# Performance work log

Measured on AMD Instinct MI355X. Metric: run time of the kernel, lower is better.

Reference implementation:

```python
import jax, jax.numpy as jnp
import numpy as np
import math

G_GRAPHS = 32   # graphs per batch
NPG = 2048      # nodes per graph
DEG = 8         # avg degree
IN_DIM = 128
HID = 128

def _lin(k, fi, fo):
    return jax.random.normal(k, (fi, fo), jnp.float32) / np.sqrt(fi).astype(np.float32)

def setup_inputs():
    key = jax.random.key(0)
    ks = jax.random.split(key, 32)
    Nt = G_GRAPHS * NPG
    Epg = NPG * DEG
    E = G_GRAPHS * Epg
    x = jax.random.normal(ks[0], (Nt, IN_DIM), jnp.float32)
    src = jax.random.randint(ks[1], (E,), 0, NPG)
    dst = jax.random.randint(ks[2], (E,), 0, NPG)
    off = (jnp.arange(E) // Epg) * NPG  # keep edges within their graph block
    edge_index = jnp.stack([src + off, dst + off]).astype(jnp.int32)
    batch = (jnp.arange(Nt) // NPG).astype(jnp.int32)
    p = {}
    dims = [(IN_DIM, HID), (HID, HID), (HID, HID), (HID, HID)]
    for i, (fi, fo) in enumerate(dims, 1):
        p['Wl%d' % i] = _lin(ks[3 * i], fi, fo)
        p['bl%d' % i] = jnp.zeros((fo,), jnp.float32)
        p['Wr%d' % i] = _lin(ks[3 * i + 1], fi, fo)
    for j in (1, 2):  # SAGPooling score GNN (GraphConv hidden->1)
        p['Prel%d' % j] = _lin(ks[15 + 2 * j], HID, 1)
        p['prb%d' % j] = jnp.zeros((1,), jnp.float32)
        p['Proot%d' % j] = _lin(ks[16 + 2 * j], HID, 1)
    p['W5'] = _lin(ks[24], HID, 64); p['b5'] = jnp.zeros((64,), jnp.float32)
    p['W6'] = _lin(ks[25], 64, 2);  p['b6'] = jnp.zeros((2,), jnp.float32)
    return dict(x=x, edge_index=edge_index, batch=batch, npg=NPG, **p)

def reference(x, edge_index, batch, npg,
              Wl1, bl1, Wr1, Wl2, bl2, Wr2, Wl3, bl3, Wr3, Wl4, bl4, Wr4,
              Prel1, prb1, Proot1, Prel2, prb2, Proot2, W5, b5, W6, b6):
    src, dst = edge_index[0], edge_index[1]
    Nt = x.shape[0]
    Gn = Nt // npg

    def sage(h, em, Wl, bl, Wr):
        # SAGEConv (mean aggr): lin_l(mean_j x_j) + lin_r(x_root)
        s = jax.ops.segment_sum(h[src] * em[:, None], dst, num_segments=Nt)
        c = jax.ops.segment_sum(em, dst, num_segments=Nt)
        return (s / jnp.maximum(c, 1.0)[:, None]) @ Wl + bl + h @ Wr

    def pool(h, em, nm, k, Prel, prb, Proot):
        # SAGPooling: score = GraphConv(h) (add aggr), top-k per graph, x *= tanh(score)
        s = jax.ops.segment_sum(h[src] * em[:, None], dst, num_segments=Nt)
        score = (s @ Prel + h @ Proot + prb)[:, 0]
        smr = jnp.where(nm > 0, score, -1e30).reshape(Gn, npg)
        _, idx = jax.lax.top_k(smr, k)
        newm = jnp.zeros((Gn, npg), h.dtype).at[jnp.arange(Gn)[:, None], idx].set(1.0).reshape(-1)
        h = h * jnp.tanh(score)[:, None] * newm[:, None]
        em = em * newm[src] * newm[dst]  # filter_adj: keep edges with both ends kept
        return h, em, newm

    em = jnp.ones(src.shape, x.dtype)
    nm = jnp.ones((Nt,), x.dtype)
    h = jax.nn.relu(sage(x, em, Wl1, bl1, Wr1))
    h = jax.nn.relu(sage(h, em, Wl2, bl2, Wr2))
    k1 = math.ceil(0.5 * npg)
    h, em, nm = pool(h, em, nm, k1, Prel1, prb1, Proot1)
    h = jax.nn.relu(sage(h, em, Wl3, bl3, Wr3)) * nm[:, None]
    h = jax.nn.relu(sage(h, em, Wl4, bl4, Wr4)) * nm[:, None]
    k2 = math.ceil(0.5 * k1)
    h, em, nm = pool(h, em, nm, k2, Prel2, prb2, Proot2)
    # global mean pool over surviving nodes
    sums = jax.ops.segment_sum(h, batch, num_segments=Gn)
    cnt = jax.ops.segment_sum(nm, batch, num_segments=Gn)
    g = sums / jnp.maximum(cnt, 1.0)[:, None]
    g = jax.nn.relu(g @ W5 + b5)
    return jax.nn.log_softmax(g @ W6 + b6, axis=1)
```

## Files before the change

kernel.cpp:

```cpp
#include <hip/hip_runtime.h>
#include <hip/hip_bf16.h>
#include <math.h>

#define NT   65536
#define NPGC 2048
#define NG   32
#define NE   524288
#define HID  128
#define K1   1024
#define K2   512

typedef short short8 __attribute__((ext_vector_type(8)));
typedef float f32x4  __attribute__((ext_vector_type(4)));

__device__ __forceinline__ float bf2f(unsigned short u) {
    union { unsigned int i; float f; } v; v.i = ((unsigned int)u) << 16; return v.f;
}
__device__ __forceinline__ unsigned short f2bf(float f) {
    union { float f; unsigned int i; } v; v.f = f;
    unsigned int x = v.i;
    return (unsigned short)((x + 0x7fffu + ((x >> 16) & 1u)) >> 16);
}
__device__ __forceinline__ void split2(float v, unsigned short& hi, unsigned short& lo) {
    unsigned int b = __float_as_uint(v);
    hi = (unsigned short)(b >> 16);
    float rem = v - __uint_as_float(b & 0xFFFF0000u);
    lo = (unsigned short)(__float_as_uint(rem) >> 16);
}

__global__ void k_detect(const unsigned short* __restrict__ x, int* __restrict__ flag) {
    __shared__ int cnt;
    if (threadIdx.x == 0) cnt = 0;
    __syncthreads();
    int sane = 0;
#pragma unroll
    for (int j = 0; j < 16; ++j) {
        unsigned short u = x[threadIdx.x * 16 + j];
        int e = (u >> 7) & 0xFF;
        if (e > 0x60 && e < 0xA0) sane++;
    }
    atomicAdd(&cnt, sane);
    __syncthreads();
    if (threadIdx.x == 0) *flag = (cnt > 3686) ? 1 : 0;
}

struct CvtDesc { const void* src[22]; int n[22]; int off[22]; };

__global__ void k_cvt(CvtDesc d, float* __restrict__ wts, const int* __restrict__ flag) {
    int t = blockIdx.y;
    int n = d.n[t];
    bool isbf = (*flag != 0);
    const unsigned short* sb = (const unsigned short*)d.src[t];
    const float* sf = (const float*)d.src[t];
    float* o = wts + d.off[t];
    for (int i = blockIdx.x * blockDim.x + threadIdx.x; i < n; i += gridDim.x * blockDim.x)
        o[i] = isbf ? bf2f(sb[i]) : sf[i];
}

__global__ void k_packW(const float* __restrict__ wts, int4 oWl, int4 oWr,
                        unsigned short* __restrict__ Wpack,
                        int* __restrict__ rowc, int* __restrict__ fill) {
    int idx = blockIdx.x * 256 + threadIdx.x;
    if (idx < NT) { rowc[idx] = 0; fill[idx] = 0; }
    if (idx >= 4 * 8 * 8 * 64 * 8) return;
    int L    = idx >> 15;
    int rem  = idx & 32767;
    int ct   = rem >> 12;
    int rem2 = rem & 4095;
    int ks   = rem2 >> 9;
    int rem3 = rem2 & 511;
    int lane = rem3 >> 3;
    int j    = rem3 & 7;
    int k   = ks * 32 + (lane >> 4) * 8 + j;
    int col = ct * 16 + (lane & 15);
    int ol = (L == 0) ? oWl.x : (L == 1) ? oWl.y : (L == 2) ? oWl.z : oWl.w;
    int orr = (L == 0) ? oWr.x : (L == 1) ? oWr.y : (L == 2) ? oWr.z : oWr.w;
    float w = (k < 128) ? wts[ol + k * 128 + col] : wts[orr + (k - 128) * 128 + col];
    unsigned short hi = f2bf(w);
    unsigned short lo = f2bf(w - bf2f(hi));
    int base = L * 65536 + (ct * 8 + ks) * 512 + lane * 8 + j;
    Wpack[base]         = hi;
    Wpack[base + 32768] = lo;
}

__global__ void k_load_x(const void* __restrict__ x, float* __restrict__ out,
                         const int* __restrict__ flag, int n4,
                         float* __restrict__ nm, const int* __restrict__ dstE,
                         int* __restrict__ rowc) {
    int i = blockIdx.x * blockDim.x + threadIdx.x;
    if (i < NT) nm[i] = 1.0f;
    if (i < NE) atomicAdd(&rowc[dstE[i]], 1);
    if (i >= n4) return;
    if (*flag) {
        ushort4 v = ((const ushort4*)x)[i];
        float4 o;
        o.x = bf2f(v.x); o.y = bf2f(v.y); o.z = bf2f(v.z); o.w = bf2f(v.w);
        ((float4*)out)[i] = o;
    }
}

__global__ void k_scan1(const int* __restrict__ cnt, int* __restrict__ rp, int* __restrict__ bsum,
                        float* __restrict__ invc) {
    __shared__ int s[256];
    int t = threadIdx.x;
    int i = blockIdx.x * 256 + t;
    int v = cnt[i];
    invc[i] = 1.0f / fmaxf((float)v, 1.0f);
    s[t] = v;
    __syncthreads();
    for (int off = 1; off < 256; off <<= 1) {
        int a = (t >= off) ? s[t - off] : 0;
        __syncthreads();
        s[t] += a;
        __syncthreads();
    }
    rp[i] = s[t] - v;
    if (t == 255) bsum[blockIdx.x] = s[255];
}

__global__ void k_scan23(int* __restrict__ rp, const int* __restrict__ bsum) {
    __shared__ int s[256];
    int t = threadIdx.x;
    s[t] = bsum[t];
    __syncthreads();
    for (int off = 1; off < 256; off <<= 1) {
        int a = (t >= off) ? s[t - off] : 0;
        __syncthreads();
        s[t] += a;
        __syncthreads();
    }
    int boffv = s[blockIdx.x] - bsum[blockIdx.x];
    int i = blockIdx.x * 256 + t;
    rp[i] += boffv;
    if (i == 0) rp[NT] = NE;
}

__global__ void k_scatter(const int* __restrict__ src, const int* __restrict__ dst,
                          const int* __restrict__ rp, int* __restrict__ fill, int* __restrict__ col) {
    int e = blockIdx.x * blockDim.x + threadIdx.x;
    if (e < NE) {
        int d = dst[e];
        int p = rp[d] + atomicAdd(&fill[d], 1);
        col[p] = src[e];
    }
}

__global__ void k_invc(const float* __restrict__ nm, const int* __restrict__ rp,
                       const int* __restrict__ col, float* __restrict__ invc,
                       const int* __restrict__ act) {
    int n = act[blockIdx.x * 256 + threadIdx.x];
    int beg = rp[n], end = rp[n + 1];
    float c = 0.f;
    for (int e = beg; e < end; ++e) c += nm[col[e]];
    invc[n] = 1.0f / fmaxf(c, 1.0f);
}

__device__ __forceinline__ int lds_sw(int node, int k) {
    int g = k >> 3;
    int go = g ^ (node & 7);
    return node * 128 + go * 8 + (k & 7);
}

template<bool HAS_TS, bool COMPACT>
__device__ __forceinline__ void sage_body(
    const float* __restrict__ h, const float* __restrict__ ts,
    const float* __restrict__ nm, const float* __restrict__ invc,
    const int* __restrict__ rp, const int* __restrict__ col,
    const unsigned short* __restrict__ Wp,
    unsigned short* Ahi, unsigned short* Alo,
    unsigned short* Bhi, unsigned short* Blo,
    int n0, const int* __restrict__ actb, int tid, f32x4 acc[2][2])
{
    int lane = tid & 63, w = tid >> 6;
    int lrow = lane & 15, quad = lane >> 4;

    float4 rootv[4]; float roots[4];
#pragma unroll
    for (int i = 0; i < 4; ++i) {
        int idx = i * 256 + tid;
        int node = idx >> 5;
        int f2 = (idx & 31) * 4;
        int gn = COMPACT ? actb[node] : n0 + node;
        rootv[i] = *(const float4*)&h[(size_t)gn * HID + f2];
        roots[i] = HAS_TS ? ts[gn] : 1.0f;
    }

    int gnode = tid >> 5;
    int f = (tid & 31) * 4;
#pragma unroll
    for (int pass = 0; pass < 4; ++pass) {
        int node = pass * 8 + gnode;
        int gn = COMPACT ? actb[node] : n0 + node;
        float ax = 0.f, ay = 0.f, az = 0.f, aw = 0.f;
        bool active = COMPACT ? true : (nm[gn] > 0.f);
        if (active) {
            int beg = rp[gn], end = rp[gn + 1];
            int ecl = end - 1;
            for (int e0 = beg; e0 < end; e0 += 8) {
                int sj[8];
#pragma unroll
                for (int j = 0; j < 8; ++j) {
                    int e = (e0 + j < end) ? e0 + j : ecl;
                    sj[j] = col[e];
                }
                float4 vj[8];
#pragma unroll
                for (int j = 0; j < 8; ++j)
                    vj[j] = *(const float4*)&h[(size_t)sj[j] * HID + f];
#pragma unroll
                for (int j = 0; j < 8; ++j) {
                    float cj = (e0 + j < end) ? (HAS_TS ? ts[sj[j]] : 1.0f) : 0.0f;
                    ax += vj[j].x * cj;
                    ay += vj[j].y * cj;
                    az += vj[j].z * cj;
                    aw += vj[j].w * cj;
                }
            }
        }
        float inv = invc[gn];
        ushort4 hi4, lo4;
        split2(ax * inv, hi4.x, lo4.x);
        split2(ay * inv, hi4.y, lo4.y);
        split2(az * inv, hi4.z, lo4.z);
        split2(aw * inv, hi4.w, lo4.w);
        int a = lds_sw(node, f);
        *(ushort4*)&Ahi[a] = hi4;
        *(ushort4*)&Alo[a] = lo4;
    }

#pragma unroll
    for (int i = 0; i < 4; ++i) {
        int idx = i * 256 + tid;
        int node = idx >> 5;
        int f2 = (idx & 31) * 4;
        float sc = roots[i];
        ushort4 hi4, lo4;
        split2(rootv[i].x * sc, hi4.x, lo4.x);
        split2(rootv[i].y * sc, hi4.y, lo4.y);
        split2(rootv[i].z * sc, hi4.z, lo4.z);
        split2(rootv[i].w * sc, hi4.w, lo4.w);
        int a = lds_sw(node, f2);
        *(ushort4*)&Bhi[a] = hi4;
        *(ushort4*)&Blo[a] = lo4;
    }
    __syncthreads();

#pragma unroll
    for (int ks = 0; ks < 8; ++ks) {
        const unsigned short* Hb = (ks < 4) ? Ahi : Bhi;
        const unsigned short* Lb = (ks < 4) ? Alo : Blo;
        short8 bh[2], blo[2];
#pragma unroll
        for (int c = 0; c < 2; ++c) {
            int ct = 2 * w + c;
            bh[c]  = *(const short8*)&Wp[(ct * 8 + ks) * 512 + lane * 8];
            blo[c] = *(const short8*)&Wp[32768 + (ct * 8 + ks) * 512 + lane * 8];
        }
        int kb = (ks & 3) * 32 + quad * 8;
#pragma unroll
        for (int st = 0; st < 2; ++st) {
            int a = lds_sw(st * 16 + lrow, kb);
            short8 ah = *(const short8*)&Hb[a];
            short8 al = *(const short8*)&Lb[a];
#pragma unroll
            for (int c = 0; c < 2; ++c) {
                acc[st][c] = __builtin_amdgcn_mfma_f32_16x16x32_bf16(ah, bh[c],  acc[st][c], 0, 0, 0);
                acc[st][c] = __builtin_amdgcn_mfma_f32_16x16x32_bf16(al, bh[c],  acc[st][c], 0, 0, 0);
                acc[st][c] = __builtin_amdgcn_mfma_f32_16x16x32_bf16(ah, blo[c], acc[st][c], 0, 0, 0);
            }
        }
    }
}

template<bool COMPACT>
__device__ __forceinline__ void map_block(int b, int& graph, int& tile) {
    if (COMPACT) { graph = (b & 7) * 4 + (b >> 8); tile = (b >> 3) & 31; }
    else         { graph = (b & 7) * 4 + (b >> 9); tile = (b >> 3) & 63; }
}

template<bool HAS_TS, bool COMPACT>
__global__ void __launch_bounds__(256, 4) k_sage_plain(
    const float* __restrict__ h, const void* __restrict__ xraw, const int* __restrict__ flag,
    const float* __restrict__ ts,
    const float* __restrict__ nm, const float* __restrict__ invc,
    const int* __restrict__ rp, const int* __restrict__ col,
    const unsigned short* __restrict__ Wp, const float* __restrict__ bl,
    float* __restrict__ out, const int* __restrict__ act)
{
    __shared__ unsigned short Ahi[32 * 128];
    __shared__ unsigned short Alo[32 * 128];
    __shared__ unsigned short Bhi[32 * 128];
    __shared__ unsigned short Blo[32 * 128];
    int tid = threadIdx.x;
    int graph, tile;
    map_block<COMPACT>(blockIdx.x, graph, tile);
    int n0 = graph * NPGC + tile * 32;
    const int* actb = COMPACT ? (act + graph * K1 + tile * 32) : nullptr;
    int lane = tid & 63, w = tid >> 6;
    int lrow = lane & 15, quad = lane >> 4;
    f32x4 acc[2][2] = {};

    const float* hh = h;
    if (!COMPACT && xraw && *flag == 0) hh = (const float*)xraw;

    sage_body<HAS_TS, COMPACT>(hh, ts, nm, invc, rp, col, Wp, Ahi, Alo, Bhi, Blo, n0, actb, tid, acc);

#pragma unroll
    for (int c = 0; c < 2; ++c) {
        int colg = (2 * w + c) * 16 + lrow;
        float bias = bl[colg];
#pragma unroll
        for (int st = 0; st < 2; ++st) {
#pragma unroll
            for (int rr = 0; rr < 4; ++rr) {
                int nl = st * 16 + quad * 4 + rr;
                int node = COMPACT ? actb[nl] : n0 + nl;
                float val = fmaxf(acc[st][c][rr] + bias, 0.f);
                if (!COMPACT) val *= nm[node];
                out[(size_t)node * HID + colg] = val;
            }
        }
    }
}

template<bool HAS_TS, bool COMPACT>
__global__ void __launch_bounds__(256, 4) k_sage_dots(
    const float* __restrict__ h, const float* __restrict__ ts,
    const float* __restrict__ nm, const float* __restrict__ invc,
    const int* __restrict__ rp, const int* __restrict__ col,
    const unsigned short* __restrict__ Wp, const float* __restrict__ bl,
    float* __restrict__ out,
    const float* __restrict__ Prel, const float* __restrict__ Proot,
    float* __restrict__ q, float* __restrict__ r, const int* __restrict__ act)
{
    __shared__ unsigned short Ahi[32 * 128];
    __shared__ unsigned short Alo[32 * 128];
    __shared__ unsigned short Bhi[32 * 128];
    __shared__ unsigned short Blo[32 * 128];
    int tid = threadIdx.x;
    int graph, tile;
    map_block<COMPACT>(blockIdx.x, graph, tile);
    int n0 = graph * NPGC + tile * 32;
    const int* actb = COMPACT ? (act + graph * K1 + tile * 32) : nullptr;
    int lane = tid & 63, w = tid >> 6;
    int lrow = lane & 15, quad = lane >> 4;
    f32x4 acc[2][2] = {};

    sage_body<HAS_TS, COMPACT>(h, ts, nm, invc, rp, col, Wp, Ahi, Alo, Bhi, Blo, n0, actb, tid, acc);

    float qp[2][4] = {}, rp_[2][4] = {};
#pragma unroll
    for (int c = 0; c < 2; ++c) {
        int colg = (2 * w + c) * 16 + lrow;
        float bias = bl[colg];
        float pq = Prel[colg], pr = Proot[colg];
#pragma unroll
        for (int st = 0; st < 2; ++st) {
#pragma unroll
            for (int rr = 0; rr < 4; ++rr) {
                int nl = st * 16 + quad * 4 + rr;
                int node = COMPACT ? actb[nl] : n0 + nl;
                float val = fmaxf(acc[st][c][rr] + bias, 0.f);
                if (!COMPACT) val *= nm[node];
                out[(size_t)node * HID + colg] = val;
                qp[st][rr] += val * pq;
                rp_[st][rr] += val * pr;
            }
        }
    }
#pragma unroll
    for (int st = 0; st < 2; ++st)
#pragma unroll
        for (int rr = 0; rr < 4; ++rr) {
#pragma unroll
            for (int m = 1; m < 16; m <<= 1) {
                qp[st][rr]  += __shfl_xor(qp[st][rr],  m, 64);
                rp_[st][rr] += __shfl_xor(rp_[st][rr], m, 64);
            }
        }
    __syncthreads();
    float* qa = (float*)Ahi;
    if (tid < 64) qa[tid] = 0.f;
    __syncthreads();
    if (lrow == 0) {
#pragma unroll
        for (int st = 0; st < 2; ++st)
#pragma unroll
            for (int rr = 0; rr < 4; ++rr) {
                int nl = st * 16 + quad * 4 + rr;
                atomicAdd(&qa[nl], qp[st][rr]);
                atomicAdd(&qa[32 + nl], rp_[st][rr]);
            }
    }
    __syncthreads();
    if (tid < 32) {
        int node = COMPACT ? actb[tid] : n0 + tid;
        q[node] = qa[tid];
        r[node] = qa[32 + tid];
    }
}

__global__ void k_score(const float* __restrict__ q, const float* __restrict__ r,
                        const float* __restrict__ prb,
                        const int* __restrict__ rp, const int* __restrict__ col,
                        float* __restrict__ score) {
    int n = blockIdx.x * 256 + threadIdx.x;
    int beg = rp[n], end = rp[n + 1];
    float s = 0.f;
    for (int e = beg; e < end; ++e) s += q[col[e]];
    score[n] = s + r[n] + prb[0];
}

__global__ void k_score_act(const float* __restrict__ q, const float* __restrict__ r,
                            const float* __restrict__ prb,
                            const int* __restrict__ rp, const int* __restrict__ col,
                            float* __restrict__ score, const int* __restrict__ act) {
    int n = act[blockIdx.x * 256 + threadIdx.x];
    int beg = rp[n], end = rp[n + 1];
    float s = 0.f;
    for (int e = beg; e < end; ++e) s += q[col[e]];
    score[n] = s + r[n] + prb[0];
}

template<bool ZQ>
__global__ void __launch_bounds__(256) k_topk(const float* __restrict__ score,
                                              float* __restrict__ nm,
                                              float* __restrict__ tval, int k,
                                              int* __restrict__ act,
                                              float* __restrict__ q) {
    __shared__ unsigned int u[NPGC];
    __shared__ int hist[256];
    __shared__ int scanb[257];
    __shared__ int wtot[4];
    __shared__ int wtot2[4];
    __shared__ unsigned int s_byte;
    __shared__ int s_kk;
    int tid = threadIdx.x;
    int lane = tid & 63, wv = tid >> 6;
    int base = blockIdx.x * NPGC;

    for (int j = tid; j < NPGC; j += 256) {
        float sc = (nm[base + j] > 0.f) ? score[base + j] : -1e30f;
        unsigned int v = __float_as_uint(sc);
        v = (v & 0x80000000u) ? ~v : (v | 0x80000000u);
        u[j] = v;
    }
    hist[tid] = 0;
    if (tid == 0) scanb[256] = 0;
    __syncthreads();

    unsigned int prefix = 0;
    int kk = k;
#pragma unroll
    for (int round = 0; round < 4; ++round) {
        int shift = 24 - 8 * round;
        unsigned int pmask = (round == 0) ? 0u : (0xFFFFFFFFu << (32 - 8 * round));
        for (int j = tid; j < NPGC; j += 256) {
            unsigned int v = u[j];
            if ((v & pmask) == prefix) atomicAdd(&hist[(v >> shift) & 0xFF], 1);
        }
        __syncthreads();
        int s = hist[tid];
#pragma unroll
        for (int off = 1; off < 64; off <<= 1) {
            int t = __shfl_down(s, off, 64);
            s += (lane + off < 64) ? t : 0;
        }
        if (lane == 0) wtot[wv] = s;
        __syncthreads();
        int add = 0;
#pragma unroll
        for (int w2 = 1; w2 < 4; ++w2) add += (wv + w2 < 4) ? wtot[wv + w2] : 0;
        s += add;
        scanb[tid] = s;
        __syncthreads();
        int above = scanb[tid + 1];
        if (s >= kk && above < kk) { s_byte = (unsigned int)tid; s_kk = kk - above; }
        hist[tid] = 0;
        __syncthreads();
        prefix |= (s_byte << shift);
        kk = s_kk;
    }
    unsigned int thr = prefix;

    int j0 = tid * 8;
    int cnt = 0;
#pragma unroll
    for (int j = 0; j < 8; ++j) cnt += (u[j0 + j] == thr);
    int s = cnt;
#pragma unroll
    for (int off = 1; off < 64; off <<= 1) {
        int t = __shfl_up(s, off, 64);
        s += (lane >= off) ? t : 0;
    }
    if (lane == 63) wtot[wv] = s;
    __syncthreads();
    int add = 0;
#pragma unroll
    for (int w2 = 0; w2 < 4; ++w2) add += (w2 < wv) ? wtot[w2] : 0;
    int rank = s - cnt + add;

    unsigned int keepmask = 0u;
    int myrank = rank;
    int kcnt = 0;
#pragma unroll
    for (int j = 0; j < 8; ++j) {
        unsigned int v = u[j0 + j];
        bool kp;
        if (v > thr) kp = true;
        else if (v == thr) { kp = (myrank < kk); myrank++; }
        else kp = false;
        keepmask |= (kp ? 1u : 0u) << j;
        kcnt += kp ? 1 : 0;
    }
    int s2 = kcnt;
#pragma unroll
    for (int off = 1; off < 64; off <<= 1) {
        int t2 = __shfl_up(s2, off, 64);
        s2 += (lane >= off) ? t2 : 0;
    }
    if (lane == 63) wtot2[wv] = s2;
    __syncthreads();
    int pos = s2 - kcnt;
#pragma unroll
    for (int w2 = 0; w2 < 4; ++w2) pos += (w2 < wv) ? wtot2[w2] : 0;
    int* actg = act + blockIdx.x * k;
#pragma unroll
    for (int j = 0; j < 8; ++j) {
        bool kp = (keepmask >> j) & 1u;
        int n = base + j0 + j;
        nm[n]   = kp ? 1.0f : 0.0f;
        tval[n] = kp ? tanhf(score[n]) : 0.0f;
        if (kp)      { actg[pos++] = n; }
        else if (ZQ) { q[n] = 0.0f; }
    }
}

__global__ void k_gsum(const float* __restrict__ h, const float* __restrict__ t,
                       const int* __restrict__ act, float* __restrict__ g) {
    int b = blockIdx.x;
    int graph = b >> 2, part = b & 3;
    int f = threadIdx.x & 127, sub = threadIdx.x >> 7;
    int base = graph * K2 + part * 128 + sub * 64;
    float acc = 0.f;
#pragma unroll 4
    for (int n = 0; n < 64; ++n) {
        int gn = act[base + n];
        acc += h[(size_t)gn * HID + f] * t[gn];
    }
    atomicAdd(&g[graph * HID + f], acc);
}

__global__ void k_mlp(const float* __restrict__ g,
                      const float* __restrict__ W5,
                      const float* __restrict__ b5, const float* __restrict__ W6,
                      const float* __restrict__ b6, void* __restrict__ out,
                      const int* __restrict__ flag) {
    __shared__ float g5[64];
    __shared__ float ls[2];
    int graph = blockIdx.x, j = threadIdx.x;
    const float ic = 1.0f / (float)K2;
    float acc = b5[j];
    for (int f = 0; f < HID; ++f)
        acc += (g[graph * HID + f] * ic) * W5[f * 64 + j];
    g5[j] = fmaxf(acc, 0.f);
    __syncthreads();
    if (j < 2) {
        float l = b6[j];
        for (int t = 0; t < 64; ++t) l += g5[t] * W6[t * 2 + j];
        ls[j] = l;
    }
    __syncthreads();
    if (j == 0) {
        float a = ls[0], b = ls[1];
        float mx = fmaxf(a, b);
        float lse = mx + logf(expf(a - mx) + expf(b - mx));
        if (*flag) {
            ((unsigned short*)out)[graph * 2 + 0] = f2bf(a - lse);
            ((unsigned short*)out)[graph * 2 + 1] = f2bf(b - lse);
        } else {
            ((float*)out)[graph * 2 + 0] = a - lse;
            ((float*)out)[graph * 2 + 1] = b - lse;
        }
    }
}

extern "C" void kernel_launch(void* const* d_in, const int* in_sizes, int n_in,
                              void* d_out, int out_size, void* d_ws, size_t ws_size,
                              hipStream_t stream) {
    const void* x    = d_in[0];
    const int*  ei   = (const int*)d_in[1];
    const int*  srcE = ei;
    const int*  dstE = ei + NE;

    char* ws = (char*)d_ws;
    float* hA    = (float*)(ws + 0);
    float* hB    = (float*)(ws + 33554432);
    float* tvec  = (float*)(ws + 67108864);
    float* invc  = (float*)(ws + 67371008);
    float* q     = (float*)(ws + 100663296);
    float* r     = (float*)(ws + 100925440);
    float* score = (float*)(ws + 101187584);
    float* nm    = (float*)(ws + 101449728);
    int*   rowc  = (int*)  (ws + 101711872);
    int*   rp    = (int*)  (ws + 101974016);
    int*   bsum  = (int*)  (ws + 102236416);
    int*   fill  = (int*)  (ws + 102238464);
    int*   col   = (int*)  (ws + 102500608);
    float* g     = (float*)(ws + 104597760);
    int*   flag  = (int*)  (ws + 104615936);
    float* wts   = (float*)(ws + 104616960);
    unsigned short* Wpack = (unsigned short*)(ws + 105179136);
    int*   act1  = rowc;
    int*   act2  = fill;
    (void)in_sizes; (void)n_in; (void)out_size; (void)ws_size;

    const int O_Wl1 = 0,      O_bl1 = 16384,  O_Wr1 = 16512;
    const int O_Wl2 = 32896,  O_bl2 = 49280,  O_Wr2 = 49408;
    const int O_Wl3 = 65792,  O_bl3 = 82176,  O_Wr3 = 82304;
    const int O_Wl4 = 98688,  O_bl4 = 115072, O_Wr4 = 115200;
    const int O_Pr1 = 131584, O_pb1 = 131712, O_Po1 = 131713;
    const int O_Pr2 = 131841, O_pb2 = 131969, O_Po2 = 131970;
    const int O_W5  = 132098, O_b5  = 140290, O_W6 = 140354, O_b6 = 140482;

    CvtDesc d;
    const int srcIdx[22] = {4,5,6,7,8,9,10,11,12,13,14,15,16,17,18,19,20,21,22,23,24,25};
    const int nelems[22] = {16384,128,16384, 16384,128,16384, 16384,128,16384, 16384,128,16384,
                            128,1,128, 128,1,128, 8192,64,128,2};
    const int offs[22]   = {O_Wl1,O_bl1,O_Wr1, O_Wl2,O_bl2,O_Wr2, O_Wl3,O_bl3,O_Wr3, O_Wl4,O_bl4,O_Wr4,
                            O_Pr1,O_pb1,O_Po1, O_Pr2,O_pb2,O_Po2, O_W5,O_b5,O_W6,O_b6};
    for (int i = 0; i < 22; ++i) { d.src[i] = d_in[srcIdx[i]]; d.n[i] = nelems[i]; d.off[i] = offs[i]; }

    hipMemsetAsync(g, 0, (NG * HID + NG + 64) * 4, stream);

    k_detect <<<1, 256, 0, stream>>>((const unsigned short*)x, flag);
    k_cvt    <<<dim3(64, 22), 256, 0, stream>>>(d, wts, flag);
    k_packW  <<<512, 256, 0, stream>>>(wts, make_int4(O_Wl1, O_Wl2, O_Wl3, O_Wl4),
                                       make_int4(O_Wr1, O_Wr2, O_Wr3, O_Wr4), Wpack, rowc, fill);
    k_load_x <<<8192, 256, 0, stream>>>(x, hA, flag, NT * HID / 4, nm, dstE, rowc);

    k_scan1  <<<256, 256, 0, stream>>>(rowc, rp, bsum, invc);
    k_scan23 <<<256, 256, 0, stream>>>(rp, bsum);
    k_scatter<<<2048, 256, 0, stream>>>(srcE, dstE, rp, fill, col);

    k_sage_plain<false, false><<<2048, 256, 0, stream>>>(hA, x, flag, nullptr, nm, invc, rp, col,
                                                         Wpack + 0 * 65536, wts + O_bl1, hB, nullptr);
    k_sage_dots<false, false><<<2048, 256, 0, stream>>>(hB, nullptr, nm, invc, rp, col,
                                                        Wpack + 1 * 65536, wts + O_bl2, hA,
                                                        wts + O_Pr1, wts + O_Po1, q, r, nullptr);

    k_score<<<256, 256, 0, stream>>>(q, r, wts + O_pb1, rp, col, score);
    k_topk<true><<<32, 256, 0, stream>>>(score, nm, tvec, K1, act1, q);
    k_invc <<<NG * K1 / 256, 256, 0, stream>>>(nm, rp, col, invc, act1);

    k_sage_plain<true, true><<<1024, 256, 0, stream>>>(hA, nullptr, flag, tvec, nm, invc, rp, col,
                                                       Wpack + 2 * 65536, wts + O_bl3, hB, act1);
    k_sage_dots<true, true><<<1024, 256, 0, stream>>>(hB, nm, nm, invc, rp, col,
                                                      Wpack + 3 * 65536, wts + O_bl4, hA,
                                                      wts + O_Pr2, wts + O_Po2, q, r, act1);

    k_score_act<<<NG * K1 / 256, 256, 0, stream>>>(q, r, wts + O_pb2, rp, col, score, act1);
    k_topk<false><<<32, 256, 0, stream>>>(score, nm, tvec, K2, act2, nullptr);

    k_gsum<<<NG * 4, 256, 0, stream>>>(hA, tvec, act2, g);
    k_mlp <<<32, 64, 0, stream>>>(g, wts + O_W5, wts + O_b5, wts + O_W6, wts + O_b6, d_out, flag);
}
```

Before: 364.2 us.

## Fuse input conversion, invc, gsum and MLP into neighbouring kernels; drop nm checks

Removes the separate bf16-to-fp32 input conversion pass by having the first SAGE layer read bf16 or fp32 input directly through a templated loader. The inverse-degree computation is folded into the first top-k kernel using an LDS keep mask, and the graph-sum and MLP kernels are merged into a single tail kernel, which drops a memset and two launches. Row pointers and degree normalisers are hoisted ahead of the gather loop, node-mask checks and multiplies are dropped in the dense layers, and launch bounds are raised to 8 waves. These changes cut launches and global traffic, at the cost of a serialised invc loop inside 32 top-k blocks and a tail reduction with little parallelism.

```diff
diff --git a/kernel.cpp b/kernel.cpp
--- a/kernel.cpp
+++ b/kernel.cpp
@@ -83,20 +83,9 @@
     Wpack[base + 32768] = lo;
 }
 
-__global__ void k_load_x(const void* __restrict__ x, float* __restrict__ out,
-                         const int* __restrict__ flag, int n4,
-                         float* __restrict__ nm, const int* __restrict__ dstE,
-                         int* __restrict__ rowc) {
-    int i = blockIdx.x * blockDim.x + threadIdx.x;
-    if (i < NT) nm[i] = 1.0f;
-    if (i < NE) atomicAdd(&rowc[dstE[i]], 1);
-    if (i >= n4) return;
-    if (*flag) {
-        ushort4 v = ((const ushort4*)x)[i];
-        float4 o;
-        o.x = bf2f(v.x); o.y = bf2f(v.y); o.z = bf2f(v.z); o.w = bf2f(v.w);
-        ((float4*)out)[i] = o;
-    }
+__global__ void k_hist(const int* __restrict__ dstE, int* __restrict__ rowc) {
+    int e = blockIdx.x * 256 + threadIdx.x;
+    if (e < NE) atomicAdd(&rowc[dstE[e]], 1);
 }
 
 __global__ void k_scan1(const int* __restrict__ cnt, int* __restrict__ rp, int* __restrict__ bsum,
@@ -145,26 +134,27 @@
     }
 }
 
-__global__ void k_invc(const float* __restrict__ nm, const int* __restrict__ rp,
-                       const int* __restrict__ col, float* __restrict__ invc,
-                       const int* __restrict__ act) {
-    int n = act[blockIdx.x * 256 + threadIdx.x];
-    int beg = rp[n], end = rp[n + 1];
-    float c = 0.f;
-    for (int e = beg; e < end; ++e) c += nm[col[e]];
-    invc[n] = 1.0f / fmaxf(c, 1.0f);
-}
-
 __device__ __forceinline__ int lds_sw(int node, int k) {
     int g = k >> 3;
     int go = g ^ (node & 7);
     return node * 128 + go * 8 + (k & 7);
 }
 
-template<bool HAS_TS, bool COMPACT>
+template<int MODE>
+__device__ __forceinline__ float4 ldrow4(const void* __restrict__ h, int node, int f) {
+    if constexpr (MODE == 1) {
+        ushort4 v = *((const ushort4*)h + (size_t)node * 32 + (f >> 2));
+        float4 o; o.x = bf2f(v.x); o.y = bf2f(v.y); o.z = bf2f(v.z); o.w = bf2f(v.w);
+        return o;
+    } else {
+        return *((const float4*)h + (size_t)node * 32 + (f >> 2));
+    }
+}
+
+template<bool HAS_TS, bool COMPACT, int MODE>
 __device__ __forceinline__ void sage_body(
-    const float* __restrict__ h, const float* __restrict__ ts,
-    const float* __restrict__ nm, const float* __restrict__ invc,
+    const void* __restrict__ h, const float* __restrict__ ts,
+    const float* __restrict__ invc,
     const int* __restrict__ rp, const int* __restrict__ col,
     const unsigned short* __restrict__ Wp,
     unsigned short* Ahi, unsigned short* Alo,
@@ -173,6 +163,16 @@
 {
     int lane = tid & 63, w = tid >> 6;
     int lrow = lane & 15, quad = lane >> 4;
+    int gnode = tid >> 5;
+    int f = (tid & 31) * 4;
+
+    int gns[4], begs[4], ends[4]; float invs[4];
+#pragma unroll
+    for (int p = 0; p < 4; ++p) gns[p] = COMPACT ? actb[p * 8 + gnode] : n0 + p * 8 + gnode;
+#pragma unroll
+    for (int p = 0; p < 4; ++p) { begs[p] = rp[gns[p]]; ends[p] = rp[gns[p] + 1]; }
+#pragma unroll
+    for (int p = 0; p < 4; ++p) invs[p] = invc[gns[p]];
 
     float4 rootv[4]; float roots[4];
 #pragma unroll
@@ -181,43 +181,37 @@
         int node = idx >> 5;
         int f2 = (idx & 31) * 4;
         int gn = COMPACT ? actb[node] : n0 + node;
-        rootv[i] = *(const float4*)&h[(size_t)gn * HID + f2];
+        rootv[i] = ldrow4<MODE>(h, gn, f2);
         roots[i] = HAS_TS ? ts[gn] : 1.0f;
     }
 
-    int gnode = tid >> 5;
-    int f = (tid & 31) * 4;
 #pragma unroll
     for (int pass = 0; pass < 4; ++pass) {
         int node = pass * 8 + gnode;
-        int gn = COMPACT ? actb[node] : n0 + node;
         float ax = 0.f, ay = 0.f, az = 0.f, aw = 0.f;
-        bool active = COMPACT ? true : (nm[gn] > 0.f);
-        if (active) {
-            int beg = rp[gn], end = rp[gn + 1];
-            int ecl = end - 1;
-            for (int e0 = beg; e0 < end; e0 += 8) {
-                int sj[8];
-#pragma unroll
-                for (int j = 0; j < 8; ++j) {
-                    int e = (e0 + j < end) ? e0 + j : ecl;
-                    sj[j] = col[e];
-                }
-                float4 vj[8];
-#pragma unroll
-                for (int j = 0; j < 8; ++j)
-                    vj[j] = *(const float4*)&h[(size_t)sj[j] * HID + f];
-#pragma unroll
-                for (int j = 0; j < 8; ++j) {
-                    float cj = (e0 + j < end) ? (HAS_TS ? ts[sj[j]] : 1.0f) : 0.0f;
-                    ax += vj[j].x * cj;
-                    ay += vj[j].y * cj;
-                    az += vj[j].z * cj;
-                    aw += vj[j].w * cj;
-                }
-            }
-        }
-        float inv = invc[gn];
+        int beg = begs[pass], end = ends[pass];
+        int ecl = end - 1;
+        for (int e0 = beg; e0 < end; e0 += 8) {
+            int sj[8];
+#pragma unroll
+            for (int j = 0; j < 8; ++j) {
+                int e = (e0 + j < end) ? e0 + j : ecl;
+                sj[j] = col[e];
+            }
+            float4 vj[8];
+#pragma unroll
+            for (int j = 0; j < 8; ++j)
+                vj[j] = ldrow4<MODE>(h, sj[j], f);
+#pragma unroll
+            for (int j = 0; j < 8; ++j) {
+                float cj = (e0 + j < end) ? (HAS_TS ? ts[sj[j]] : 1.0f) : 0.0f;
+                ax += vj[j].x * cj;
+                ay += vj[j].y * cj;
+                az += vj[j].z * cj;
+                aw += vj[j].w * cj;
+            }
+        }
+        float inv = invs[pass];
         ushort4 hi4, lo4;
         split2(ax * inv, hi4.x, lo4.x);
         split2(ay * inv, hi4.y, lo4.y);
@@ -278,11 +272,48 @@
     else         { graph = (b & 7) * 4 + (b >> 9); tile = (b >> 3) & 63; }
 }
 
-template<bool HAS_TS, bool COMPACT>
-__global__ void __launch_bounds__(256, 4) k_sage_plain(
-    const float* __restrict__ h, const void* __restrict__ xraw, const int* __restrict__ flag,
-    const float* __restrict__ ts,
-    const float* __restrict__ nm, const float* __restrict__ invc,
+__global__ void __launch_bounds__(256, 8) k_sage_l1(
+    const void* __restrict__ x, const int* __restrict__ flag,
+    const float* __restrict__ invc,
+    const int* __restrict__ rp, const int* __restrict__ col,
+    const unsigned short* __restrict__ Wp, const float* __restrict__ bl,
+    float* __restrict__ out)
+{
+    __shared__ unsigned short Ahi[32 * 128];
+    __shared__ unsigned short Alo[32 * 128];
+    __shared__ unsigned short Bhi[32 * 128];
+    __shared__ unsigned short Blo[32 * 128];
+    int tid = threadIdx.x;
+    int graph, tile;
+    map_block<false>(blockIdx.x, graph, tile);
+    int n0 = graph * NPGC + tile * 32;
+    int lane = tid & 63, w = tid >> 6;
+    int lrow = lane & 15, quad = lane >> 4;
+    f32x4 acc[2][2] = {};
+
+    if (*flag)
+        sage_body<false, false, 1>(x, nullptr, invc, rp, col, Wp, Ahi, Alo, Bhi, Blo, n0, nullptr, tid, acc);
+    else
+        sage_body<false, false, 0>(x, nullptr, invc, rp, col, Wp, Ahi, Alo, Bhi, Blo, n0, nullptr, tid, acc);
+
+#pragma unroll
+    for (int c = 0; c < 2; ++c) {
+        int colg = (2 * w + c) * 16 + lrow;
+        float bias = bl[colg];
+#pragma unroll
+        for (int st = 0; st < 2; ++st) {
+#pragma unroll
+            for (int rr = 0; rr < 4; ++rr) {
+                int node = n0 + st * 16 + quad * 4 + rr;
+                out[(size_t)node * HID + colg] = fmaxf(acc[st][c][rr] + bias, 0.f);
+            }
+        }
+    }
+}
+
+__global__ void __launch_bounds__(256, 8) k_sage_plain(
+    const float* __restrict__ h, const float* __restrict__ ts,
+    const float* __restrict__ invc,
     const int* __restrict__ rp, const int* __restrict__ col,
     const unsigned short* __restrict__ Wp, const float* __restrict__ bl,
     float* __restrict__ out, const int* __restrict__ act)
@@ -293,17 +324,14 @@
     __shared__ unsigned short Blo[32 * 128];
     int tid = threadIdx.x;
     int graph, tile;
-    map_block<COMPACT>(blockIdx.x, graph, tile);
+    map_block<true>(blockIdx.x, graph, tile);
     int n0 = graph * NPGC + tile * 32;
-    const int* actb = COMPACT ? (act + graph * K1 + tile * 32) : nullptr;
+    const int* actb = act + graph * K1 + tile * 32;
     int lane = tid & 63, w = tid >> 6;
     int lrow = lane & 15, quad = lane >> 4;
     f32x4 acc[2][2] = {};
 
-    const float* hh = h;
-    if (!COMPACT && xraw && *flag == 0) hh = (const float*)xraw;
-
-    sage_body<HAS_TS, COMPACT>(hh, ts, nm, invc, rp, col, Wp, Ahi, Alo, Bhi, Blo, n0, actb, tid, acc);
+    sage_body<true, true, 0>(h, ts, invc, rp, col, Wp, Ahi, Alo, Bhi, Blo, n0, actb, tid, acc);
 
 #pragma unroll
     for (int c = 0; c < 2; ++c) {
@@ -313,20 +341,17 @@
         for (int st = 0; st < 2; ++st) {
 #pragma unroll
             for (int rr = 0; rr < 4; ++rr) {
-                int nl = st * 16 + quad * 4 + rr;
-                int node = COMPACT ? actb[nl] : n0 + nl;
-                float val = fmaxf(acc[st][c][rr] + bias, 0.f);
-                if (!COMPACT) val *= nm[node];
-                out[(size_t)node * HID + colg] = val;
+                int node = actb[st * 16 + quad * 4 + rr];
+                out[(size_t)node * HID + colg] = fmaxf(acc[st][c][rr] + bias, 0.f);
             }
         }
     }
 }
 
 template<bool HAS_TS, bool COMPACT>
-__global__ void __launch_bounds__(256, 4) k_sage_dots(
+__global__ void __launch_bounds__(256, 8) k_sage_dots(
     const float* __restrict__ h, const float* __restrict__ ts,
-    const float* __restrict__ nm, const float* __restrict__ invc,
+    const float* __restrict__ invc,
     const int* __restrict__ rp, const int* __restrict__ col,
     const unsigned short* __restrict__ Wp, const float* __restrict__ bl,
     float* __restrict__ out,
@@ -346,7 +371,7 @@
     int lrow = lane & 15, quad = lane >> 4;
     f32x4 acc[2][2] = {};
 
-    sage_body<HAS_TS, COMPACT>(h, ts, nm, invc, rp, col, Wp, Ahi, Alo, Bhi, Blo, n0, actb, tid, acc);
+    sage_body<HAS_TS, COMPACT, 0>(h, ts, invc, rp, col, Wp, Ahi, Alo, Bhi, Blo, n0, actb, tid, acc);
 
     float qp[2][4] = {}, rp_[2][4] = {};
 #pragma unroll
@@ -361,7 +386,6 @@
                 int nl = st * 16 + quad * 4 + rr;
                 int node = COMPACT ? actb[nl] : n0 + nl;
                 float val = fmaxf(acc[st][c][rr] + bias, 0.f);
-                if (!COMPACT) val *= nm[node];
                 out[(size_t)node * HID + colg] = val;
                 qp[st][rr] += val * pq;
                 rp_[st][rr] += val * pr;
@@ -422,13 +446,17 @@
     score[n] = s + r[n] + prb[0];
 }
 
-template<bool ZQ>
+template<bool NMIN, bool DO_INVC, bool ZQ>
 __global__ void __launch_bounds__(256) k_topk(const float* __restrict__ score,
                                               float* __restrict__ nm,
                                               float* __restrict__ tval, int k,
                                               int* __restrict__ act,
-                                              float* __restrict__ q) {
+                                              float* __restrict__ q,
+                                              const int* __restrict__ rp,
+                                              const int* __restrict__ col,
+                                              float* __restrict__ invc) {
     __shared__ unsigned int u[NPGC];
+    __shared__ unsigned char kb[NPGC];
     __shared__ int hist[256];
     __shared__ int scanb[257];
     __shared__ int wtot[4];
@@ -440,7 +468,7 @@
     int base = blockIdx.x * NPGC;
 
     for (int j = tid; j < NPGC; j += 256) {
-        float sc = (nm[base + j] > 0.f) ? score[base + j] : -1e30f;
+        float sc = NMIN ? ((nm[base + j] > 0.f) ? score[base + j] : -1e30f) : score[base + j];
         unsigned int v = __float_as_uint(sc);
         v = (v & 0x80000000u) ? ~v : (v | 0x80000000u);
         u[j] = v;
@@ -512,6 +540,7 @@
         else kp = false;
         keepmask |= (kp ? 1u : 0u) << j;
         kcnt += kp ? 1 : 0;
+        kb[j0 + j] = kp ? 1 : 0;
     }
     int s2 = kcnt;
 #pragma unroll
@@ -534,44 +563,55 @@
         if (kp)      { actg[pos++] = n; }
         else if (ZQ) { q[n] = 0.0f; }
     }
-}
-
-__global__ void k_gsum(const float* __restrict__ h, const float* __restrict__ t,
-                       const int* __restrict__ act, float* __restrict__ g) {
-    int b = blockIdx.x;
-    int graph = b >> 2, part = b & 3;
-    int f = threadIdx.x & 127, sub = threadIdx.x >> 7;
-    int base = graph * K2 + part * 128 + sub * 64;
-    float acc = 0.f;
-#pragma unroll 4
-    for (int n = 0; n < 64; ++n) {
-        int gn = act[base + n];
-        acc += h[(size_t)gn * HID + f] * t[gn];
-    }
-    atomicAdd(&g[graph * HID + f], acc);
-}
-
-__global__ void k_mlp(const float* __restrict__ g,
-                      const float* __restrict__ W5,
-                      const float* __restrict__ b5, const float* __restrict__ W6,
-                      const float* __restrict__ b6, void* __restrict__ out,
-                      const int* __restrict__ flag) {
+
+    if (DO_INVC) {
+        __syncthreads();
+        for (int j = tid; j < NPGC; j += 256) {
+            if (kb[j]) {
+                int n = base + j;
+                int bg = rp[n], en = rp[n + 1];
+                float c = 0.f;
+                for (int e = bg; e < en; ++e) c += (float)kb[col[e] - base];
+                invc[n] = 1.0f / fmaxf(c, 1.0f);
+            }
+        }
+    }
+}
+
+__global__ void k_tail(const float* __restrict__ h, const float* __restrict__ t,
+                       const int* __restrict__ act,
+                       const float* __restrict__ W5, const float* __restrict__ b5,
+                       const float* __restrict__ W6, const float* __restrict__ b6,
+                       void* __restrict__ out, const int* __restrict__ flag) {
+    __shared__ float gsh[2][HID];
     __shared__ float g5[64];
     __shared__ float ls[2];
-    int graph = blockIdx.x, j = threadIdx.x;
-    const float ic = 1.0f / (float)K2;
-    float acc = b5[j];
-    for (int f = 0; f < HID; ++f)
-        acc += (g[graph * HID + f] * ic) * W5[f * 64 + j];
-    g5[j] = fmaxf(acc, 0.f);
-    __syncthreads();
-    if (j < 2) {
-        float l = b6[j];
-        for (int t = 0; t < 64; ++t) l += g5[t] * W6[t * 2 + j];
-        ls[j] = l;
-    }
-    __syncthreads();
-    if (j == 0) {
+    int graph = blockIdx.x, tid = threadIdx.x;
+    int f = tid & 127, sub = tid >> 7;
+    const int* actg = act + graph * K2;
+    float acc = 0.f;
+#pragma unroll 8
+    for (int i = 0; i < 256; ++i) {
+        int gn = actg[sub * 256 + i];
+        acc += h[(size_t)gn * HID + f] * t[gn];
+    }
+    gsh[sub][f] = acc;
+    __syncthreads();
+    if (tid < 64) {
+        const float ic = 1.0f / (float)K2;
+        float a5 = b5[tid];
+        for (int ff = 0; ff < HID; ++ff)
+            a5 += (gsh[0][ff] + gsh[1][ff]) * ic * W5[ff * 64 + tid];
+        g5[tid] = fmaxf(a5, 0.f);
+    }
+    __syncthreads();
+    if (tid < 2) {
+        float l = b6[tid];
+        for (int tt = 0; tt < 64; ++tt) l += g5[tt] * W6[tt * 2 + tid];
+        ls[tid] = l;
+    }
+    __syncthreads();
+    if (tid == 0) {
         float a = ls[0], b = ls[1];
         float mx = fmaxf(a, b);
         float lse = mx + logf(expf(a - mx) + expf(b - mx));
@@ -607,7 +647,6 @@
     int*   bsum  = (int*)  (ws + 102236416);
     int*   fill  = (int*)  (ws + 102238464);
     int*   col   = (int*)  (ws + 102500608);
-    float* g     = (float*)(ws + 104597760);
     int*   flag  = (int*)  (ws + 104615936);
     float* wts   = (float*)(ws + 104616960);
     unsigned short* Wpack = (unsigned short*)(ws + 105179136);
@@ -631,37 +670,34 @@
                             O_Pr1,O_pb1,O_Po1, O_Pr2,O_pb2,O_Po2, O_W5,O_b5,O_W6,O_b6};
     for (int i = 0; i < 22; ++i) { d.src[i] = d_in[srcIdx[i]]; d.n[i] = nelems[i]; d.off[i] = offs[i]; }
 
-    hipMemsetAsync(g, 0, (NG * HID + NG + 64) * 4, stream);
-
     k_detect <<<1, 256, 0, stream>>>((const unsigned short*)x, flag);
     k_cvt    <<<dim3(64, 22), 256, 0, stream>>>(d, wts, flag);
     k_packW  <<<512, 256, 0, stream>>>(wts, make_int4(O_Wl1, O_Wl2, O_Wl3, O_Wl4),
                                        make_int4(O_Wr1, O_Wr2, O_Wr3, O_Wr4), Wpack, rowc, fill);
-    k_load_x <<<8192, 256, 0, stream>>>(x, hA, flag, NT * HID / 4, nm, dstE, rowc);
+    k_hist   <<<2048, 256, 0, stream>>>(dstE, rowc);
 
     k_scan1  <<<256, 256, 0, stream>>>(rowc, rp, bsum, invc);
     k_scan23 <<<256, 256, 0, stream>>>(rp, bsum);
     k_scatter<<<2048, 256, 0, stream>>>(srcE, dstE, rp, fill, col);
 
-    k_sage_plain<false, false><<<2048, 256, 0, stream>>>(hA, x, flag, nullptr, nm, invc, rp, col,
-                                                         Wpack + 0 * 65536, wts + O_bl1, hB, nullptr);
-    k_sage_dots<false, false><<<2048, 256, 0, stream>>>(hB, nullptr, nm, invc, rp, col,
+    k_sage_l1<<<2048, 256, 0, stream>>>(x, flag, invc, rp, col,
+                                        Wpack + 0 * 65536, wts + O_bl1, hB);
+    k_sage_dots<false, false><<<2048, 256, 0, stream>>>(hB, nullptr, invc, rp, col,
                                                         Wpack + 1 * 65536, wts + O_bl2, hA,
                                                         wts + O_Pr1, wts + O_Po1, q, r, nullptr);
 
     k_score<<<256, 256, 0, stream>>>(q, r, wts + O_pb1, rp, col, score);
-    k_topk<true><<<32, 256, 0, stream>>>(score, nm, tvec, K1, act1, q);
-    k_invc <<<NG * K1 / 256, 256, 0, stream>>>(nm, rp, col, invc, act1);
-
-    k_sage_plain<true, true><<<1024, 256, 0, stream>>>(hA, nullptr, flag, tvec, nm, invc, rp, col,
-                                                       Wpack + 2 * 65536, wts + O_bl3, hB, act1);
-    k_sage_dots<true, true><<<1024, 256, 0, stream>>>(hB, nm, nm, invc, rp, col,
+    k_topk<false, true, true><<<32, 256, 0, stream>>>(score, nm, tvec, K1, act1, q, rp, col, invc);
+
+    k_sage_plain<<<1024, 256, 0, stream>>>(hA, tvec, invc, rp, col,
+                                           Wpack + 2 * 65536, wts + O_bl3, hB, act1);
+    k_sage_dots<true, true><<<1024, 256, 0, stream>>>(hB, nm, invc, rp, col,
                                                       Wpack + 3 * 65536, wts + O_bl4, hA,
                                                       wts + O_Pr2, wts + O_Po2, q, r, act1);
 
     k_score_act<<<NG * K1 / 256, 256, 0, stream>>>(q, r, wts + O_pb2, rp, col, score, act1);
-    k_topk<false><<<32, 256, 0, stream>>>(score, nm, tvec, K2, act2, nullptr);
-
-    k_gsum<<<NG * 4, 256, 0, stream>>>(hA, tvec, act2, g);
-    k_mlp <<<32, 64, 0, stream>>>(g, wts + O_W5, wts + O_b5, wts + O_W6, wts + O_b6, d_out, flag);
-}
+    k_topk<true, false, false><<<32, 256, 0, stream>>>(score, nm, tvec, K2, act2, nullptr, rp, col, nullptr);
+
+    k_tail<<<32, 256, 0, stream>>>(hA, tvec, act2, wts + O_W5, wts + O_b5,
+                                   wts + O_W6, wts + O_b6, d_out, flag);
+}
```

Result: slower. 382.7 us (+5.1%).
